# Optimization experiments

Measured on AMD Instinct MI355X. Metric: run time of the kernel, lower is better.

Reference implementation:

```python
import jax, jax.numpy as jnp
import numpy as np

B, T, C, H = 1, 4096, 768, 12
D = C // H  # head_dim = 64


def setup_inputs() -> dict:
    key = jax.random.key(0)
    ks = jax.random.split(key, 5)
    s = 1.0 / np.sqrt(C)
    return {
        "x": jax.random.normal(ks[0], (B, T, C), dtype=jnp.float32),
        "Wq": jax.random.normal(ks[1], (C, C), dtype=jnp.float32) * s,
        "bq": jnp.zeros((C,), dtype=jnp.float32),
        "Wk": jax.random.normal(ks[2], (C, C), dtype=jnp.float32) * s,
        "bk": jnp.zeros((C,), dtype=jnp.float32),
        "Wv": jax.random.normal(ks[3], (C, C), dtype=jnp.float32) * s,
        "bv": jnp.zeros((C,), dtype=jnp.float32),
        "Wo": jax.random.normal(ks[4], (C, C), dtype=jnp.float32) * s,
        "bo": jnp.zeros((C,), dtype=jnp.float32),
    }


def reference(x, Wq, bq, Wk, bk, Wv, bv, Wo, bo):
    # Linear projections (torch nn.Linear: y = x @ W.T + b)
    q = (x @ Wq.T + bq).reshape(B, T, H, D).transpose(0, 2, 1, 3)  # [B,H,T,D]
    k = (x @ Wk.T + bk).reshape(B, T, H, D).transpose(0, 2, 1, 3)
    v = (x @ Wv.T + bv).reshape(B, T, H, D).transpose(0, 2, 1, 3)
    scale = 1.0 / jnp.sqrt(jnp.asarray(D, dtype=x.dtype))
    scores = jnp.einsum("bhqd,bhkd->bhqk", q, k) * scale  # [B,H,T,T]
    attn = jax.nn.softmax(scores, axis=-1)
    out = jnp.einsum("bhqk,bhkd->bhqd", attn, v)  # [B,H,T,D]
    y = out.transpose(0, 2, 1, 3).reshape(B, T, C)
    return y @ Wo.T + bo
```

## Files before the change

### kernel.cpp

```cpp
#include <hip/hip_runtime.h>
#include <math.h>

#define T_ 4096
#define C_ 768
#define H_ 12
#define D_ 64
#define TC_ ((size_t)T_ * C_)
#define CC_ ((size_t)C_ * C_)

typedef __attribute__((ext_vector_type(8))) __bf16 bf16x8;
typedef __attribute__((ext_vector_type(4))) __bf16 bf16x4;
typedef __attribute__((ext_vector_type(2))) __bf16 bf16x2;
typedef __attribute__((ext_vector_type(4))) float f32x4;
typedef __attribute__((ext_vector_type(16))) float f32x16;
typedef __attribute__((ext_vector_type(8))) unsigned short u16x8;
typedef __attribute__((ext_vector_type(4))) unsigned int u32x4;

#define MFIX 24.0f

static __device__ __forceinline__ float fast_exp2(float x) {
#if __has_builtin(__builtin_amdgcn_exp2f)
    return __builtin_amdgcn_exp2f(x);
#else
    return exp2f(x);
#endif
}

static __device__ __forceinline__ unsigned pack2(float a, float b) {
    bf16x2 v = { (__bf16)a, (__bf16)b };
    return __builtin_bit_cast(unsigned, v);
}

static __device__ __forceinline__ void gload16(const void* g, void* l) {
    __builtin_amdgcn_global_load_lds(
        (const __attribute__((address_space(1))) unsigned int*)g,
        (__attribute__((address_space(3))) unsigned int*)l, 16, 0, 0);
}

__global__ void f2b_kernel(const float* __restrict__ in,
                           unsigned short* __restrict__ out, int n4) {
    int i = blockIdx.x * blockDim.x + threadIdx.x;
    const int stride = gridDim.x * blockDim.x;
    for (; i < n4; i += stride) {
        float4 v = ((const float4*)in)[i];
        bf16x4 o = { (__bf16)v.x, (__bf16)v.y, (__bf16)v.z, (__bf16)v.w };
        *(bf16x4*)&out[(size_t)i * 4] = o;
    }
}

__global__ void f2b4_kernel(const float* __restrict__ w0, const float* __restrict__ w1,
                            const float* __restrict__ w2, const float* __restrict__ w3,
                            unsigned short* __restrict__ out) {
    const float* src = (blockIdx.y == 0) ? w0 : (blockIdx.y == 1) ? w1
                     : (blockIdx.y == 2) ? w2 : w3;
    unsigned short* dst = out + (size_t)blockIdx.y * CC_;
    const int i = blockIdx.x * blockDim.x + threadIdx.x;
    float4 v = ((const float4*)src)[i];
    bf16x4 o = { (__bf16)v.x, (__bf16)v.y, (__bf16)v.z, (__bf16)v.w };
    *(bf16x4*)&dst[(size_t)i * 4] = o;
}

#define BM 128
#define BN 128
#define BKG 64

struct GemmRegs {
    const unsigned short* ag[4];
    const unsigned short* wg[4];
    unsigned short* la[4];
    unsigned short* lw[4];
    int lq, lg, wr, wc;
};

static __device__ __forceinline__ void gemm_setup(
    GemmRegs& R, const unsigned short* A, const unsigned short* W,
    unsigned short* Asm, unsigned short* Bsm, int bm, int bn, int K)
{
    const int tid = threadIdx.x;
    const int wave = tid >> 6, lane = tid & 63;
    R.lq = lane & 15; R.lg = lane >> 4;
    R.wr = wave >> 1; R.wc = wave & 1;
#pragma unroll
    for (int i = 0; i < 4; ++i) {
        const int flat = wave * 256 + i * 64 + lane;
        const int row = flat >> 3, cb = flat & 7;
        R.ag[i] = A + (size_t)(bm + row) * K + cb * 8;
        R.wg[i] = W + (size_t)(bn + row) * K + cb * 8;
        R.la[i] = Asm + (wave * 4 + i) * 512;
        R.lw[i] = Bsm + (wave * 4 + i) * 512;
    }
}

static __device__ __forceinline__ void gemm_loop(
    GemmRegs& R, unsigned short* Asm, unsigned short* Bsm, int K, f32x4 acc[4][4])
{
    for (int kb = 0; kb < K; kb += BKG) {
        __syncthreads();
#pragma unroll
        for (int i = 0; i < 4; ++i) {
            gload16(R.ag[i] + kb, R.la[i]);
            gload16(R.wg[i] + kb, R.lw[i]);
        }
        __syncthreads();
        __builtin_amdgcn_s_setprio(1);
#pragma unroll
        for (int ks = 0; ks < 2; ++ks) {
            bf16x8 af[4], wf[4];
#pragma unroll
            for (int m = 0; m < 4; ++m)
                af[m] = *(const bf16x8*)&Asm[(R.wr * 64 + m * 16 + R.lq) * BKG + ks * 32 + R.lg * 8];
#pragma unroll
            for (int n = 0; n < 4; ++n)
                wf[n] = *(const bf16x8*)&Bsm[(R.wc * 64 + n * 16 + R.lq) * BKG + ks * 32 + R.lg * 8];
#pragma unroll
            for (int m = 0; m < 4; ++m)
#pragma unroll
                for (int n = 0; n < 4; ++n)
                    acc[m][n] = __builtin_amdgcn_mfma_f32_16x16x32_bf16(af[m], wf[n], acc[m][n], 0, 0, 0);
        }
        __builtin_amdgcn_s_setprio(0);
    }
}

__global__ __launch_bounds__(256) void qkv128(
    const unsigned short* __restrict__ xb,
    const unsigned short* __restrict__ Wqb, const unsigned short* __restrict__ Wkb,
    const unsigned short* __restrict__ Wvb,
    const float* __restrict__ bq, const float* __restrict__ bk, const float* __restrict__ bv,
    unsigned short* __restrict__ Qb, unsigned short* __restrict__ Kb,
    unsigned short* __restrict__ Vtb)
{
    __shared__ unsigned short Asm[BM * BKG];
    __shared__ unsigned short Bsm[BN * BKG];
    const int z = blockIdx.z;
    const unsigned short* W = (z == 0) ? Wqb : (z == 1) ? Wkb : Wvb;
    const float* bias = (z == 0) ? bq : (z == 1) ? bk : bv;
    const int bm = blockIdx.x * BM, bn = blockIdx.y * BN;

    GemmRegs R;
    gemm_setup(R, xb, W, Asm, Bsm, bm, bn, C_);
    f32x4 acc[4][4] = {};
    gemm_loop(R, Asm, Bsm, C_, acc);

    const float sc = (z == 0) ? 0.18033688011112042f : 1.0f;
#pragma unroll
    for (int mt = 0; mt < 4; ++mt) {
        const int m0 = bm + R.wr * 64 + mt * 16 + R.lg * 4;
#pragma unroll
        for (int nt = 0; nt < 4; ++nt) {
            const int n = bn + R.wc * 64 + nt * 16 + R.lq;
            const float b = bias[n];
            if (z == 2) {
                bf16x4 o = { (__bf16)(acc[mt][nt][0] + b), (__bf16)(acc[mt][nt][1] + b),
                             (__bf16)(acc[mt][nt][2] + b), (__bf16)(acc[mt][nt][3] + b) };
                *(bf16x4*)&Vtb[(size_t)n * T_ + m0] = o;
            } else {
                unsigned short* Y = (z == 0) ? Qb : Kb;
#pragma unroll
                for (int r = 0; r < 4; ++r)
                    Y[(size_t)(m0 + r) * C_ + n] =
                        __builtin_bit_cast(unsigned short, (__bf16)((acc[mt][nt][r] + b) * sc));
            }
        }
    }
}

__global__ __launch_bounds__(256) void out128(
    const unsigned short* __restrict__ ctxb, const unsigned short* __restrict__ Wob,
    const float* __restrict__ bo, float* __restrict__ out)
{
    __shared__ unsigned short Asm[BM * BKG];
    __shared__ unsigned short Bsm[BN * BKG];
    const int bm = blockIdx.x * BM, bn = blockIdx.y * BN;

    GemmRegs R;
    gemm_setup(R, ctxb, Wob, Asm, Bsm, bm, bn, C_);
    f32x4 acc[4][4] = {};
    gemm_loop(R, Asm, Bsm, C_, acc);

#pragma unroll
    for (int mt = 0; mt < 4; ++mt) {
        const int m0 = bm + R.wr * 64 + mt * 16 + R.lg * 4;
#pragma unroll
        for (int nt = 0; nt < 4; ++nt) {
            const int n = bn + R.wc * 64 + nt * 16 + R.lq;
            const float b = bo[n];
#pragma unroll
            for (int r = 0; r < 4; ++r)
                out[(size_t)(m0 + r) * C_ + n] = acc[mt][nt][r] + b;
        }
    }
}

#define SPLITS 2
#define KVTILES (T_ / 64 / SPLITS)

__global__ __launch_bounds__(256, 3) void attn32s(
    const unsigned short* __restrict__ Qb, const unsigned short* __restrict__ Kb,
    const unsigned short* __restrict__ Vtb, unsigned short* __restrict__ Opart,
    float* __restrict__ lpart)
{
    __shared__ unsigned short Ks[64 * 64];
    __shared__ unsigned short Vs[64 * 64];

    const int tid = threadIdx.x;
    const int wave = tid >> 6, lane = tid & 63;
    const int lq = lane & 31, hi = lane >> 5;

    const int bid = blockIdx.x;
    const int sw = (bid & 7) * 96 + (bid >> 3);
    const int split = sw / 384;
    const int rem = sw - split * 384;
    const int h = rem >> 5, qt = rem & 31;
    const int q0 = qt * 128 + wave * 32;
    const int kv0 = split * (T_ / SPLITS);

    const int swz = (lq & 7) << 4;
    int rof[4];
#pragma unroll
    for (int ks = 0; ks < 4; ++ks)
        rof[ks] = lq * 128 + ((hi * 16 + ks * 32) ^ swz);

    bf16x8 qf[4];
    {
        const unsigned short* qp = Qb + (size_t)(q0 + lq) * C_ + h * D_ + hi * 8;
#pragma unroll
        for (int ks = 0; ks < 4; ++ks) qf[ks] = *(const bf16x8*)(qp + ks * 16);
    }

    const char* gk[2];
    const char* gv[2];
    char* kds[2];
    char* vds[2];
#pragma unroll
    for (int j = 0; j < 2; ++j) {
        const int f = j * 256 + tid;
        const int row = f >> 3;
        const int col = (f & 7) * 16;
        gk[j] = (const char*)Kb + (size_t)(kv0 + row) * (C_ * 2) + h * (D_ * 2) + col;
        gv[j] = (const char*)Vtb + (size_t)(h * D_ + row) * (T_ * 2) + kv0 * 2 + col;
        kds[j] = (char*)Ks + row * 128 + (col ^ ((row & 7) << 4));
        vds[j] = (char*)Vs + row * 128 + (col ^ ((row & 7) << 4));
    }

    u16x8 kreg[2], vreg[2];
#pragma unroll
    for (int j = 0; j < 2; ++j) {
        kreg[j] = *(const u16x8*)(gk[j]);
        vreg[j] = *(const u16x8*)(gv[j]);
    }

    f32x16 oacc0 = {}, oacc1 = {};
    float lrun = 0.f;

    for (int it = 0; it < KVTILES; ++it) {
        __syncthreads();
#pragma unroll
        for (int j = 0; j < 2; ++j) {
            *(u16x8*)kds[j] = kreg[j];
            *(u16x8*)vds[j] = vreg[j];
        }
        __syncthreads();

        if (it + 1 < KVTILES) {
            const size_t ko = (size_t)(it + 1) * 64 * (C_ * 2);
            const size_t vo = (size_t)(it + 1) * 128;
#pragma unroll
            for (int j = 0; j < 2; ++j) {
                kreg[j] = *(const u16x8*)(gk[j] + ko);
                vreg[j] = *(const u16x8*)(gv[j] + vo);
            }
        }

        const char* kb = (const char*)&Ks[0];
        const char* vb = (const char*)&Vs[0];

        f32x16 s0 = {}, s1 = {};
        __builtin_amdgcn_s_setprio(1);
#pragma unroll
        for (int ks = 0; ks < 4; ++ks) {
            bf16x8 kf0 = *(const bf16x8*)(kb + rof[ks]);
            bf16x8 kf1 = *(const bf16x8*)(kb + 4096 + rof[ks]);
            s0 = __builtin_amdgcn_mfma_f32_32x32x16_bf16(kf0, qf[ks], s0, 0, 0, 0);
            s1 = __builtin_amdgcn_mfma_f32_32x32x16_bf16(kf1, qf[ks], s1, 0, 0, 0);
        }
        __builtin_amdgcn_s_setprio(0);

#pragma unroll
        for (int r = 0; r < 16; ++r) {
            s0[r] = fast_exp2(s0[r] - MFIX);
            s1[r] = fast_exp2(s1[r] - MFIX);
        }
        {
            float ps[8];
#pragma unroll
            for (int r = 0; r < 8; ++r)
                ps[r] = (s0[r] + s0[r + 8]) + (s1[r] + s1[r + 8]);
            ps[0] += ps[4]; ps[1] += ps[5]; ps[2] += ps[6]; ps[3] += ps[7];
            float pt = (ps[0] + ps[1]) + (ps[2] + ps[3]);
            lrun += pt + __shfl_xor(pt, 32);
        }

        bf16x8 pf[4];
#pragma unroll
        for (int half = 0; half < 2; ++half) {
            const f32x16& s = half ? s1 : s0;
            unsigned g[8];
#pragma unroll
            for (int a = 0; a < 8; ++a) g[a] = pack2(s[2 * a], s[2 * a + 1]);
            unsigned V0 = hi ? g[0] : g[2];
            unsigned V1 = hi ? g[1] : g[3];
            unsigned xV0 = __shfl_xor((int)V0, 32);
            unsigned xV1 = __shfl_xor((int)V1, 32);
            u32x4 pk0 = { hi ? xV0 : g[0], hi ? xV1 : g[1],
                          hi ? g[2] : xV0, hi ? g[3] : xV1 };
            pf[2 * half + 0] = __builtin_bit_cast(bf16x8, pk0);
            unsigned W0 = hi ? g[4] : g[6];
            unsigned W1 = hi ? g[5] : g[7];
            unsigned xW0 = __shfl_xor((int)W0, 32);
            unsigned xW1 = __shfl_xor((int)W1, 32);
            u32x4 pk1 = { hi ? xW0 : g[4], hi ? xW1 : g[5],
                          hi ? g[6] : xW0, hi ? g[7] : xW1 };
            pf[2 * half + 1] = __builtin_bit_cast(bf16x8, pk1);
        }

        __builtin_amdgcn_s_setprio(1);
#pragma unroll
        for (int ks = 0; ks < 4; ++ks) {
            bf16x8 vf0 = *(const bf16x8*)(vb + rof[ks]);
            bf16x8 vf1 = *(const bf16x8*)(vb + 4096 + rof[ks]);
            oacc0 = __builtin_amdgcn_mfma_f32_32x32x16_bf16(vf0, pf[ks], oacc0, 0, 0, 0);
            oacc1 = __builtin_amdgcn_mfma_f32_32x32x16_bf16(vf1, pf[ks], oacc1, 0, 0, 0);
        }
        __builtin_amdgcn_s_setprio(0);
    }

    unsigned short* op = Opart + ((size_t)(split * H_ + h) * T_ + q0 + lq) * 64;
#pragma unroll
    for (int k = 0; k < 4; ++k) {
        bf16x4 o0 = { (__bf16)oacc0[4 * k + 0], (__bf16)oacc0[4 * k + 1],
                      (__bf16)oacc0[4 * k + 2], (__bf16)oacc0[4 * k + 3] };
        *(bf16x4*)&op[8 * k + 4 * hi] = o0;
        bf16x4 o1 = { (__bf16)oacc1[4 * k + 0], (__bf16)oacc1[4 * k + 1],
                      (__bf16)oacc1[4 * k + 2], (__bf16)oacc1[4 * k + 3] };
        *(bf16x4*)&op[32 + 8 * k + 4 * hi] = o1;
    }
    if (hi == 0)
        lpart[(size_t)(split * H_ + h) * T_ + q0 + lq] = lrun;
}

__global__ __launch_bounds__(256) void combine2(
    const unsigned short* __restrict__ Opart, const float* __restrict__ lpart,
    unsigned short* __restrict__ ctxb)
{
    const int idx = blockIdx.x * 256 + threadIdx.x;
    const int dq = idx & 15;
    const int ht = idx >> 4;
    const int h = ht >> 12;
    const int t = ht & (T_ - 1);

    const float l0 = lpart[(size_t)h * T_ + t];
    const float l1 = lpart[(size_t)(H_ + h) * T_ + t];
    const float inv = 1.f / (l0 + l1);
    const bf16x4 a0 = *(const bf16x4*)&Opart[((size_t)h * T_ + t) * 64 + dq * 4];
    const bf16x4 a1 = *(const bf16x4*)&Opart[((size_t)(H_ + h) * T_ + t) * 64 + dq * 4];
    bf16x4 r;
#pragma unroll
    for (int i = 0; i < 4; ++i)
        r[i] = (__bf16)(((float)a0[i] + (float)a1[i]) * inv);
    *(bf16x4*)&ctxb[(size_t)t * C_ + h * D_ + dq * 4] = r;
}

extern "C" void kernel_launch(void* const* d_in, const int* in_sizes, int n_in,
                              void* d_out, int out_size, void* d_ws, size_t ws_size,
                              hipStream_t stream) {
    (void)in_sizes; (void)n_in; (void)out_size; (void)ws_size;
    const float* x  = (const float*)d_in[0];
    const float* Wq = (const float*)d_in[1];
    const float* bq = (const float*)d_in[2];
    const float* Wk = (const float*)d_in[3];
    const float* bk = (const float*)d_in[4];
    const float* Wv = (const float*)d_in[5];
    const float* bv = (const float*)d_in[6];
    const float* Wo = (const float*)d_in[7];
    const float* bo = (const float*)d_in[8];
    float* out = (float*)d_out;

    unsigned short* ws    = (unsigned short*)d_ws;
    unsigned short* xb    = ws;
    unsigned short* Wqb   = xb + TC_;
    unsigned short* Wkb   = Wqb + CC_;
    unsigned short* Wvb   = Wkb + CC_;
    unsigned short* Wob   = Wvb + CC_;
    unsigned short* Qb    = Wob + CC_;
    unsigned short* Kb    = Qb + TC_;
    unsigned short* Vtb   = Kb + TC_;
    unsigned short* ctxb  = Vtb + TC_;
    unsigned short* Opart = ctxb + TC_;
    float* lpart = (float*)(Opart + 2 * TC_);

    f2b_kernel<<<2048, 256, 0, stream>>>(x, xb, (int)(TC_ / 4));
    dim3 gw(CC_ / 4 / 256, 4);
    f2b4_kernel<<<gw, 256, 0, stream>>>(Wq, Wk, Wv, Wo, Wqb);

    dim3 gq(T_ / BM, C_ / BN, 3);
    qkv128<<<gq, 256, 0, stream>>>(xb, Wqb, Wkb, Wvb, bq, bk, bv, Qb, Kb, Vtb);

    attn32s<<<768, 256, 0, stream>>>(Qb, Kb, Vtb, Opart, lpart);
    combine2<<<(T_ * H_ * 16) / 256, 256, 0, stream>>>(Opart, lpart, ctxb);

    dim3 go(T_ / BM, C_ / BN);
    out128<<<go, 256, 0, stream>>>(ctxb, Wob, bo, out);
}
```

Before: 134.2 us.

## Double-buffer attention K/V LDS tiles and swizzle GEMM LDS layout

The attention kernel now keeps two LDS buffers for K and V. The next tile is written into the idle buffer after the compute on the current one, so each iteration needs one barrier instead of two, and the register prefetch runs two tiles ahead. Separately, the projection GEMM permutes the global-load column (XOR by row) and applies the matching XOR on the LDS fragment reads, which is meant to cut LDS bank conflicts. The double buffer doubles the attention LDS footprint, which may lower occupancy under the 3-blocks launch bound.

```diff
diff --git a/kernel.cpp b/kernel.cpp
--- a/kernel.cpp
+++ b/kernel.cpp
@@ -83,9 +83,10 @@
 #pragma unroll
     for (int i = 0; i < 4; ++i) {
         const int flat = wave * 256 + i * 64 + lane;
-        const int row = flat >> 3, cb = flat & 7;
-        R.ag[i] = A + (size_t)(bm + row) * K + cb * 8;
-        R.wg[i] = W + (size_t)(bn + row) * K + cb * 8;
+        const int row = flat >> 3;
+        const int col = ((flat & 7) * 8) ^ ((row & 7) << 3);
+        R.ag[i] = A + (size_t)(bm + row) * K + col;
+        R.wg[i] = W + (size_t)(bn + row) * K + col;
         R.la[i] = Asm + (wave * 4 + i) * 512;
         R.lw[i] = Bsm + (wave * 4 + i) * 512;
     }
@@ -94,6 +95,13 @@
 static __device__ __forceinline__ void gemm_loop(
     GemmRegs& R, unsigned short* Asm, unsigned short* Bsm, int K, f32x4 acc[4][4])
 {
+    const int sw = (R.lq & 7) << 3;
+    int colA[2], colB[2];
+#pragma unroll
+    for (int ks = 0; ks < 2; ++ks) {
+        colA[ks] = (ks * 32 + R.lg * 8) ^ sw;
+        colB[ks] = colA[ks];
+    }
     for (int kb = 0; kb < K; kb += BKG) {
         __syncthreads();
 #pragma unroll
@@ -108,10 +116,10 @@
             bf16x8 af[4], wf[4];
 #pragma unroll
             for (int m = 0; m < 4; ++m)
-                af[m] = *(const bf16x8*)&Asm[(R.wr * 64 + m * 16 + R.lq) * BKG + ks * 32 + R.lg * 8];
+                af[m] = *(const bf16x8*)&Asm[(R.wr * 64 + m * 16 + R.lq) * BKG + colA[ks]];
 #pragma unroll
             for (int n = 0; n < 4; ++n)
-                wf[n] = *(const bf16x8*)&Bsm[(R.wc * 64 + n * 16 + R.lq) * BKG + ks * 32 + R.lg * 8];
+                wf[n] = *(const bf16x8*)&Bsm[(R.wc * 64 + n * 16 + R.lq) * BKG + colB[ks]];
 #pragma unroll
             for (int m = 0; m < 4; ++m)
 #pragma unroll
@@ -200,8 +208,8 @@
     const unsigned short* __restrict__ Vtb, unsigned short* __restrict__ Opart,
     float* __restrict__ lpart)
 {
-    __shared__ unsigned short Ks[64 * 64];
-    __shared__ unsigned short Vs[64 * 64];
+    __shared__ unsigned short Ks[2][64 * 64];
+    __shared__ unsigned short Vs[2][64 * 64];
 
     const int tid = threadIdx.x;
     const int wave = tid >> 6, lane = tid & 63;
@@ -239,8 +247,8 @@
         const int col = (f & 7) * 16;
         gk[j] = (const char*)Kb + (size_t)(kv0 + row) * (C_ * 2) + h * (D_ * 2) + col;
         gv[j] = (const char*)Vtb + (size_t)(h * D_ + row) * (T_ * 2) + kv0 * 2 + col;
-        kds[j] = (char*)Ks + row * 128 + (col ^ ((row & 7) << 4));
-        vds[j] = (char*)Vs + row * 128 + (col ^ ((row & 7) << 4));
+        kds[j] = (char*)&Ks[0][0] + row * 128 + (col ^ ((row & 7) << 4));
+        vds[j] = (char*)&Vs[0][0] + row * 128 + (col ^ ((row & 7) << 4));
     }
 
     u16x8 kreg[2], vreg[2];
@@ -249,31 +257,25 @@
         kreg[j] = *(const u16x8*)(gk[j]);
         vreg[j] = *(const u16x8*)(gv[j]);
     }
+#pragma unroll
+    for (int j = 0; j < 2; ++j) {
+        *(u16x8*)kds[j] = kreg[j];
+        *(u16x8*)vds[j] = vreg[j];
+    }
+    __syncthreads();
+#pragma unroll
+    for (int j = 0; j < 2; ++j) {
+        kreg[j] = *(const u16x8*)(gk[j] + 64 * (C_ * 2));
+        vreg[j] = *(const u16x8*)(gv[j] + 128);
+    }
 
     f32x16 oacc0 = {}, oacc1 = {};
     float lrun = 0.f;
 
     for (int it = 0; it < KVTILES; ++it) {
-        __syncthreads();
-#pragma unroll
-        for (int j = 0; j < 2; ++j) {
-            *(u16x8*)kds[j] = kreg[j];
-            *(u16x8*)vds[j] = vreg[j];
-        }
-        __syncthreads();
-
-        if (it + 1 < KVTILES) {
-            const size_t ko = (size_t)(it + 1) * 64 * (C_ * 2);
-            const size_t vo = (size_t)(it + 1) * 128;
-#pragma unroll
-            for (int j = 0; j < 2; ++j) {
-                kreg[j] = *(const u16x8*)(gk[j] + ko);
-                vreg[j] = *(const u16x8*)(gv[j] + vo);
-            }
-        }
-
-        const char* kb = (const char*)&Ks[0];
-        const char* vb = (const char*)&Vs[0];
+        const int cur = it & 1;
+        const char* kb = (const char*)&Ks[cur][0];
+        const char* vb = (const char*)&Vs[cur][0];
 
         f32x16 s0 = {}, s1 = {};
         __builtin_amdgcn_s_setprio(1);
@@ -333,6 +335,25 @@
             oacc1 = __builtin_amdgcn_mfma_f32_32x32x16_bf16(vf1, pf[ks], oacc1, 0, 0, 0);
         }
         __builtin_amdgcn_s_setprio(0);
+
+        if (it + 1 < KVTILES) {
+            const int nxt = (cur ^ 1) * 8192;
+#pragma unroll
+            for (int j = 0; j < 2; ++j) {
+                *(u16x8*)(kds[j] + nxt) = kreg[j];
+                *(u16x8*)(vds[j] + nxt) = vreg[j];
+            }
+            if (it + 2 < KVTILES) {
+                const size_t ko = (size_t)(it + 2) * 64 * (C_ * 2);
+                const size_t vo = (size_t)(it + 2) * 128;
+#pragma unroll
+                for (int j = 0; j < 2; ++j) {
+                    kreg[j] = *(const u16x8*)(gk[j] + ko);
+                    vreg[j] = *(const u16x8*)(gv[j] + vo);
+                }
+            }
+        }
+        __syncthreads();
     }
 
     unsigned short* op = Opart + ((size_t)(split * H_ + h) * T_ + q0 + lq) * 64;
```

Measured after the change: 126.7 us. 1.06x faster.
